# Performance work log

Hardware: AMD Instinct MI355X
Metric: run time of the kernel (lower is better)

## Reference

```python
import jax, jax.numpy as jnp
import numpy as np


def _quant(x):
    # Per-tensor dynamic uint8 quantization to produce LUT row/col indices.
    # (The CUDA kernel's exact requant scheme is not in the source; this is the
    # assumed scheme: scale so max |x| -> 255, round, clip to [0,255].)
    s = 255.0 / jnp.maximum(jnp.max(jnp.abs(x)), jnp.float32(1e-6))
    return jnp.clip(jnp.round(x * s), 0, 255).astype(jnp.int32)


def _lut_conv(x, w, b, lut):
    # CustomAnyConv2d: stride=1, padding=(2,2), kernel 5x5.
    O, Cin, kh, kw = w.shape
    # im2col patches: (B, Cin*kh*kw, H, W), feature ordering matches w.reshape(O, -1)
    patches = jax.lax.conv_general_dilated_patches(
        x, (kh, kw), (1, 1), ((2, 2), (2, 2)))
    B, K, H, W = patches.shape
    pi = _quant(patches).reshape(B, K, H * W)            # (B,K,P)
    wi = _quant(w.reshape(O, K))                          # (O,K)
    vals = lut[pi[:, None, :, :], wi[None, :, :, None]]   # (B,O,K,P) gather
    out = vals.sum(axis=2).reshape(B, O, H, W)            # accumulate LUT products
    return out + b[None, :, None, None]


def _lut_dense(x, w, b, lut):
    # CustomAnyDense: out[h, o] = sum_k LUT[x[h,k], w[o,k]] + b[o]
    xi = _quant(x)                                        # (B,K)
    wi = _quant(w)                                        # (O,K)
    vals = lut[xi[:, None, :], wi[None, :, :]]            # (B,O,K)
    return vals.sum(axis=2) + b


def _maxpool2(x, pad=0):
    return jax.lax.reduce_window(
        x, -jnp.inf, jax.lax.max,
        (1, 1, 2, 2), (1, 1, 2, 2),
        ((0, 0), (0, 0), (pad, pad), (pad, pad)))


def setup_inputs() -> dict:
    key = jax.random.key(0)
    ks = jax.random.split(key, 11)
    B = 32
    x = jax.random.uniform(ks[0], (B, 1, 28, 28), jnp.float32)
    ij = np.arange(256)
    # Approximate-multiplier LUT: high byte of exact 8x8-bit product (uint8-valued).
    lut = jnp.asarray(((ij[:, None] * ij[None, :]) >> 8).astype(np.float32))
    return {
        "x": x,
        "lut": lut,
        "w1": jax.random.uniform(ks[1], (16, 1, 5, 5), jnp.float32),
        "b1": jax.random.normal(ks[2], (16,), jnp.float32) * 0.01,
        "w2": jax.random.uniform(ks[3], (32, 16, 5, 5), jnp.float32),
        "b2": jax.random.normal(ks[4], (32,), jnp.float32) * 0.01,
        "w3": jax.random.uniform(ks[5], (64, 32, 5, 5), jnp.float32),
        "b3": jax.random.normal(ks[6], (64,), jnp.float32) * 0.01,
        "fw1": jax.random.uniform(ks[7], (256, 1024), jnp.float32),
        "fb1": jax.random.normal(ks[8], (256,), jnp.float32) * 0.01,
        "fw2": jax.random.uniform(ks[9], (10, 256), jnp.float32),
        "fb2": jax.random.normal(ks[10], (10,), jnp.float32) * 0.01,
    }


def reference(x, lut, w1, b1, w2, b2, w3, b3, fw1, fb1, fw2, fb2):
    h = jax.nn.relu(_lut_conv(x, w1, b1, lut))
    h = _maxpool2(h)                     # (B,16,14,14)
    h = jax.nn.relu(_lut_conv(h, w2, b2, lut))
    h = _maxpool2(h)                     # (B,32,7,7)
    h = jax.nn.relu(_lut_conv(h, w3, b3, lut))
    h = _maxpool2(h, pad=1)              # (B,64,4,4)
    h = h.reshape(h.shape[0], -1)        # (B,1024)
    h = jax.nn.relu(_lut_dense(h, fw1, fb1, lut))
    h = _lut_dense(h, fw2, fb2, lut)     # (B,10)
    return jax.nn.log_softmax(h, axis=1)
```

## Files before the change

### kernel.cpp

```cpp
#include <hip/hip_runtime.h>
#include <math.h>

typedef unsigned int  u32;
typedef unsigned long long u64;
typedef unsigned short u16;
typedef unsigned short u16x2 __attribute__((ext_vector_type(2)));

#define O_A1     4096
#define O_A2     405504
#define O_A3     606208
#define O_A4     737280
#define O_BARB   770048
#define BAR_WORDS 4224
#define O_FW1Q   790528

#define NBLK     512u

__device__ __forceinline__ float ldf(const float* p) {
  return __hip_atomic_load(p, __ATOMIC_RELAXED, __HIP_MEMORY_SCOPE_AGENT);
}
__device__ __forceinline__ void stf(float* p, float v) {
  __hip_atomic_store(p, v, __ATOMIC_RELAXED, __HIP_MEMORY_SCOPE_AGENT);
}
__device__ __forceinline__ u64 ld8(const u64* p) {
  return __hip_atomic_load(p, __ATOMIC_RELAXED, __HIP_MEMORY_SCOPE_AGENT);
}
__device__ __forceinline__ void st4u(u32* p, u32 v) {
  __hip_atomic_store(p, v, __ATOMIC_RELAXED, __HIP_MEMORY_SCOPE_AGENT);
}

__device__ __forceinline__ float blk_max(float v, float* red) {
  int t = threadIdx.x;
  __syncthreads();
  red[t] = v;
  __syncthreads();
#pragma unroll
  for (int s = 128; s > 0; s >>= 1) {
    if (t < s) red[t] = fmaxf(red[t], red[t + s]);
    __syncthreads();
  }
  return red[0];
}

__device__ __forceinline__ void amax_f(float* slot, float v) {
  atomicMax((int*)slot, (int)__float_as_uint(v));
}

__device__ __forceinline__ u16 quant1(float v, float s) {
  float q = rintf(v * s);
  q = fminf(fmaxf(q, 0.0f), 255.0f);
  return (u16)q;
}

__device__ __forceinline__ void mac_u32(u32& acc, u32 a, u32 w) {
  u16x2 av = __builtin_bit_cast(u16x2, a);
  u16x2 wv = __builtin_bit_cast(u16x2, w);
  u16x2 p  = av * wv;
  acc += (__builtin_bit_cast(u32, p) >> 8) & 0x00FF00FFu;
}
__device__ __forceinline__ void mac4(u32& acc, uint4 a, uint4 w) {
  mac_u32(acc, a.x, w.x); mac_u32(acc, a.y, w.y);
  mac_u32(acc, a.z, w.z); mac_u32(acc, a.w, w.w);
}

__device__ __forceinline__ float fmax4(float4 v) {
  return fmaxf(fmaxf(fabsf(v.x), fabsf(v.y)), fmaxf(fabsf(v.z), fabsf(v.w)));
}

__device__ __forceinline__ void gbar(int i, u32* bb) {
  __syncthreads();
  if (threadIdx.x == 0) {
    u32* root = bb + i * 16;
    u32* flag = bb + 64;
    u32* leaf = bb + 128 + (i * 64 + (int)(blockIdx.x >> 3)) * 16;
    asm volatile("s_waitcnt vmcnt(0)" ::: "memory");
    u32 lo = __hip_atomic_fetch_add(leaf, 1u, __ATOMIC_RELAXED,
                                    __HIP_MEMORY_SCOPE_AGENT);
    if (lo == 7u) {
      u32 ro = __hip_atomic_fetch_add(root, 1u, __ATOMIC_RELAXED,
                                      __HIP_MEMORY_SCOPE_AGENT);
      if (ro == 63u)
        __hip_atomic_store(flag, (u32)(i + 1), __ATOMIC_RELAXED,
                           __HIP_MEMORY_SCOPE_AGENT);
    }
    while (__hip_atomic_load(flag, __ATOMIC_RELAXED,
                             __HIP_MEMORY_SCOPE_AGENT) < (u32)(i + 1))
      __builtin_amdgcn_s_sleep(2);
  }
  __syncthreads();
}

__global__ __launch_bounds__(256) void k_zero(u32* p) {
  for (int i = threadIdx.x; i < BAR_WORDS; i += 256) p[i] = 0;
}

__global__ __launch_bounds__(256, 2) void k_fused(
    const float* __restrict__ x,
    const float* __restrict__ w1, const float* __restrict__ b1,
    const float* __restrict__ w2, const float* __restrict__ b2,
    const float* __restrict__ w3, const float* __restrict__ b3,
    const float* __restrict__ fw1, const float* __restrict__ fb1,
    const float* __restrict__ fw2, const float* __restrict__ fb2,
    float* __restrict__ a1, float* __restrict__ a2,
    float* __restrict__ a3, float* __restrict__ a4,
    float* __restrict__ out, float* wsf) {
  __shared__ __align__(16) union {
    struct { unsigned char sx[1024]; u16 sw[64]; } c1;
    struct { u16 sa[324 * 16]; u16 sw[800]; int sconv[196]; } c2;
    struct { u16 sa3[121 * 40]; u16 sw3[3200]; } c3;
    struct { u16 sh[1024]; } d1;
    struct { u16 sh2[256]; float z[16]; } d2;
  } sm;
  __shared__ float red[256];
  const int t = threadIdx.x, bid = blockIdx.x;
  u32* bb = (u32*)((char*)wsf + O_BARB);
  u32* fw1q32 = (u32*)((char*)wsf + O_FW1Q);

  if (bid >= 256) {
    if (bid < 315) {
      int sb = bid - 256;
      const float* p; int n4, base, nb, slot;
      if (sb < 2)       { p = w2;  n4 = 3200;  base = sb;      nb = 2;  slot = 2; }
      else if (sb < 10) { p = w3;  n4 = 12800; base = sb - 2;  nb = 8;  slot = 3; }
      else if (sb < 58) { p = fw1; n4 = 65536; base = sb - 10; nb = 48; slot = 4; }
      else              { p = fw2; n4 = 640;   base = 0;       nb = 1;  slot = 5; }
      const float4* p4 = (const float4*)p;
      float m = 0.f;
      for (int i = base * 256 + t; i < n4; i += nb * 256) m = fmaxf(m, fmax4(p4[i]));
      m = blk_max(m, red);
      if (t == 0) amax_f(wsf + slot, m);
    }
  } else {
    int b = bid >> 3, op = bid & 7;
    float m = 0.f;
    const float4* x4 = (const float4*)x;
    for (int i = t; i < 6272; i += 256) m = fmaxf(m, fmax4(x4[i]));
    float xmax = blk_max(m, red);
    m = 0.f;
    if (t < 100) m = fmax4(((const float4*)w1)[t]);
    float w1max = blk_max(m, red);
    float s0  = 255.0f / fmaxf(xmax, 1e-6f);
    float sw1 = 255.0f / fmaxf(w1max, 1e-6f);

    u32* sxz = (u32*)sm.c1.sx;
    for (int i = t; i < 256; i += 256) sxz[i] = 0;
    __syncthreads();
    for (int i = t; i < 784; i += 256) {
      int y = i / 28, xx = i - y * 28;
      sm.c1.sx[(y + 2) * 32 + xx + 2] = (unsigned char)quant1(x[b * 784 + i], s0);
    }
    if (t < 50) sm.c1.sw[t] = quant1(w1[op * 50 + t], sw1);
    __syncthreads();
    float lm = 0.f;
    if (t < 196) {
      int py = t / 14, px = t - py * 14;
#pragma unroll
      for (int ol = 0; ol < 2; ++ol) {
        int oc = op * 2 + ol;
        int best = -2147483647;
#pragma unroll
        for (int dy = 0; dy < 2; ++dy)
#pragma unroll
          for (int dx = 0; dx < 2; ++dx) {
            int cy = 2 * py + dy, cx = 2 * px + dx;
            int acc = 0;
#pragma unroll
            for (int kh = 0; kh < 5; ++kh) {
              const unsigned char* xp = sm.c1.sx + (cy + kh) * 32 + cx;
#pragma unroll
              for (int kw = 0; kw < 5; ++kw)
                acc += ((int)xp[kw] * (int)sm.c1.sw[ol * 25 + kh * 5 + kw]) >> 8;
            }
            best = max(best, acc);
          }
        float v = fmaxf(0.f, (float)best + b1[oc]);
        stf(a1 + b * 3136 + t * 16 + oc, v);
        lm = fmaxf(lm, v);
      }
    }
    lm = blk_max(lm, red);
    if (t == 0) amax_f(wsf + 6, lm);
  }
  gbar(0, bb);

  {
    {
      float swsq = 255.0f / fmaxf(ldf(wsf + 4), 1e-6f);
      int i = bid * 256 + t;
      float2 f = ((const float2*)fw1)[i];
      st4u(fw1q32 + i, (u32)quant1(f.x, swsq) | ((u32)quant1(f.y, swsq) << 16));
    }
    int b = bid >> 4, og = bid & 15;
    float s1 = 255.0f / fmaxf(ldf(wsf + 6), 1e-6f);
    float sw2s = 255.0f / fmaxf(ldf(wsf + 2), 1e-6f);
    u32* sz = (u32*)sm.c2.sa;
    for (int i = t; i < 2592; i += 256) sz[i] = 0;
    __syncthreads();
    const u64* a1u = (const u64*)(a1 + b * 3136);
    for (int i2 = t; i2 < 1568; i2 += 256) {
      int px = i2 >> 3, c2 = i2 & 7;
      int y = px / 14, xx = px - y * 14;
      float2 f = __builtin_bit_cast(float2, ld8(a1u + i2));
      u32 pk = (u32)quant1(f.x, s1) | ((u32)quant1(f.y, s1) << 16);
      ((u32*)sm.c2.sa)[((y + 2) * 18 + xx + 2) * 8 + c2] = pk;
    }
    for (int i = t; i < 800; i += 256) {
      int ol = i / 400, r = i - ol * 400, c = r / 25, tp = r - c * 25;
      sm.c2.sw[ol * 400 + tp * 16 + c] = quant1(w2[(og * 2 + ol) * 400 + c * 25 + tp], sw2s);
    }
    __syncthreads();
    int h = t & 1, pxb = t >> 1;
    float lm = 0.f;
    for (int ol = 0; ol < 2; ++ol) {
      int oc = og * 2 + ol;
      const uint4* wq = (const uint4*)(sm.c2.sw + ol * 400);
#pragma unroll
      for (int rep = 0; rep < 2; ++rep) {
        int px = pxb + rep * 128;
        if (px < 196) {
          int y = px / 14, xx = px - y * 14;
          u32 acc = 0;
#pragma unroll
          for (int kh = 0; kh < 5; ++kh)
#pragma unroll
            for (int kw = 0; kw < 5; ++kw) {
              int row = (y + kh) * 18 + (xx + kw);
              uint4 av = *(const uint4*)(sm.c2.sa + row * 16 + h * 8);
              mac4(acc, av, wq[(kh * 5 + kw) * 2 + h]);
            }
          int ai = (int)((acc & 0xFFFFu) + (acc >> 16));
          ai += __shfl_down(ai, 1, 2);
          if (h == 0) sm.c2.sconv[px] = ai;
        }
      }
      __syncthreads();
      if (t < 49) {
        int py = t / 7, px = t - py * 7;
        int mm = sm.c2.sconv[(2 * py) * 14 + 2 * px];
        mm = max(mm, sm.c2.sconv[(2 * py) * 14 + 2 * px + 1]);
        mm = max(mm, sm.c2.sconv[(2 * py + 1) * 14 + 2 * px]);
        mm = max(mm, sm.c2.sconv[(2 * py + 1) * 14 + 2 * px + 1]);
        float v = fmaxf(0.f, (float)mm + b2[oc]);
        stf(a2 + b * 1568 + t * 32 + oc, v);
        lm = fmaxf(lm, v);
      }
      __syncthreads();
    }
    lm = blk_max(lm, red);
    if (t == 0) amax_f(wsf + 7, lm);
  }
  gbar(1, bb);

  {
    int b = bid >> 4, og = bid & 15;
    float s2 = 255.0f / fmaxf(ldf(wsf + 7), 1e-6f);
    float sw3s = 255.0f / fmaxf(ldf(wsf + 3), 1e-6f);
    u32* sz = (u32*)sm.c3.sa3;
    for (int i = t; i < 2420; i += 256) sz[i] = 0;
    __syncthreads();
    const u64* a2u = (const u64*)(a2 + b * 1568);
    for (int i2 = t; i2 < 784; i2 += 256) {
      int px = i2 >> 4, c2 = i2 & 15;
      int y = px / 7, xx = px - y * 7;
      float2 f = __builtin_bit_cast(float2, ld8(a2u + i2));
      u32 pk = (u32)quant1(f.x, s2) | ((u32)quant1(f.y, s2) << 16);
      ((u32*)sm.c3.sa3)[((y + 2) * 11 + xx + 2) * 20 + c2] = pk;
    }
    for (int i = t; i < 3200; i += 256) {
      int ol = i / 800, r = i - ol * 800, c = r / 25, tp = r - c * 25;
      sm.c3.sw3[ol * 800 + tp * 32 + c] = quant1(w3[(og * 4 + ol) * 800 + c * 25 + tp], sw3s);
    }
    __syncthreads();
    int q = t & 3, pos = t >> 2;
    int dydx = pos & 3, r = pos >> 2;
    int py = r >> 2, px = r & 3;
    int cy = 2 * py - 1 + (dydx >> 1), cx = 2 * px - 1 + (dydx & 1);
    bool valid = (cy >= 0 && cy < 7 && cx >= 0 && cx < 7);
    float lm = 0.f;
    for (int ol = 0; ol < 4; ++ol) {
      int oc = og * 4 + ol;
      int ai = 0;
      if (valid) {
        u32 acc = 0;
#pragma unroll
        for (int kh = 0; kh < 5; ++kh)
#pragma unroll
          for (int kw = 0; kw < 5; ++kw) {
            int row = (cy + kh) * 11 + (cx + kw);
            uint4 av = *(const uint4*)(sm.c3.sa3 + row * 40 + q * 8);
            uint4 wv = *(const uint4*)(sm.c3.sw3 + ol * 800 + (kh * 5 + kw) * 32 + q * 8);
            mac4(acc, av, wv);
          }
        ai = (int)((acc & 0xFFFFu) + (acc >> 16));
      }
      ai += __shfl_down(ai, 2, 4);
      ai += __shfl_down(ai, 1, 4);
      int val = valid ? ai : -(1 << 30);
      int mm = max(val, __shfl_down(val, 4, 16));
      mm = max(mm, __shfl_down(mm, 8, 16));
      if ((t & 15) == 0) {
        float v = fmaxf(0.f, (float)mm + b3[oc]);
        stf(a3 + b * 1024 + oc * 16 + r, v);
        lm = fmaxf(lm, v);
      }
    }
    lm = blk_max(lm, red);
    if (t == 0) amax_f(wsf + 8, lm);
  }
  gbar(2, bb);

  {
    int b = bid >> 4, og = bid & 15;
    float s3 = 255.0f / fmaxf(ldf(wsf + 8), 1e-6f);
    const u64* a3u = (const u64*)(a3 + b * 1024);
    for (int i2 = t; i2 < 512; i2 += 256) {
      float2 f = __builtin_bit_cast(float2, ld8(a3u + i2));
      ((u32*)sm.d1.sh)[i2] = (u32)quant1(f.x, s3) | ((u32)quant1(f.y, s3) << 16);
    }
    __syncthreads();
    int ol = t >> 4, ks = t & 15;
    int o = og * 16 + ol;
    const u64* wq8 = (const u64*)fw1q32 + o * 256;
    const uint4* hp = (const uint4*)sm.d1.sh;
    u32 acc = 0;
#pragma unroll
    for (int j = 0; j < 8; ++j) {
      int e = j * 16 + ks;
      u64 w01 = ld8(wq8 + e * 2), w23 = ld8(wq8 + e * 2 + 1);
      uint4 wv;
      wv.x = (u32)w01; wv.y = (u32)(w01 >> 32);
      wv.z = (u32)w23; wv.w = (u32)(w23 >> 32);
      mac4(acc, hp[e], wv);
    }
    int ai = (int)((acc & 0xFFFFu) + (acc >> 16));
#pragma unroll
    for (int d = 8; d > 0; d >>= 1)
      ai += __shfl_down(ai, d, 16);
    float lm = 0.f;
    if (ks == 0) {
      float v = fmaxf(0.f, (float)ai + fb1[o]);
      stf(a4 + b * 256 + o, v);
      lm = v;
    }
    lm = blk_max(lm, red);
    if (t == 0) amax_f(wsf + 9, lm);
  }
  gbar(3, bb);

  if (bid < 32) {
    int b = bid;
    float s4 = 255.0f / fmaxf(ldf(wsf + 9), 1e-6f);
    float sws = 255.0f / fmaxf(ldf(wsf + 5), 1e-6f);
    sm.d2.sh2[t] = quant1(ldf(a4 + b * 256 + t), s4);
    __syncthreads();
    if (t < 40) {
      int o = t >> 2, ks = t & 3;
      const float4* wf = (const float4*)(fw2 + o * 256);
      const uint4* hp = (const uint4*)sm.d2.sh2;
      u32 acc = 0;
#pragma unroll
      for (int j = 0; j < 8; ++j) {
        int e = j * 4 + ks;
        float4 f0 = wf[e * 2], f1 = wf[e * 2 + 1];
        uint4 wv;
        wv.x = (u32)quant1(f0.x, sws) | ((u32)quant1(f0.y, sws) << 16);
        wv.y = (u32)quant1(f0.z, sws) | ((u32)quant1(f0.w, sws) << 16);
        wv.z = (u32)quant1(f1.x, sws) | ((u32)quant1(f1.y, sws) << 16);
        wv.w = (u32)quant1(f1.z, sws) | ((u32)quant1(f1.w, sws) << 16);
        mac4(acc, hp[e], wv);
      }
      int ai = (int)((acc & 0xFFFFu) + (acc >> 16));
      ai += __shfl_down(ai, 2, 4);
      ai += __shfl_down(ai, 1, 4);
      if (ks == 0) sm.d2.z[o] = (float)ai + fb2[o];
    }
    __syncthreads();
    if (t < 10) {
      float mz = sm.d2.z[0];
#pragma unroll
      for (int j = 1; j < 10; ++j) mz = fmaxf(mz, sm.d2.z[j]);
      float se = 0.f;
#pragma unroll
      for (int j = 0; j < 10; ++j) se += expf(sm.d2.z[j] - mz);
      out[b * 10 + t] = sm.d2.z[t] - (mz + logf(se));
    }
  }
}

extern "C" void kernel_launch(void* const* d_in, const int* in_sizes, int n_in,
                              void* d_out, int out_size, void* d_ws, size_t ws_size,
                              hipStream_t stream) {
  const float* x   = (const float*)d_in[0];
  const float* w1  = (const float*)d_in[2];
  const float* b1  = (const float*)d_in[3];
  const float* w2  = (const float*)d_in[4];
  const float* b2  = (const float*)d_in[5];
  const float* w3  = (const float*)d_in[6];
  const float* b3  = (const float*)d_in[7];
  const float* fw1 = (const float*)d_in[8];
  const float* fb1 = (const float*)d_in[9];
  const float* fw2 = (const float*)d_in[10];
  const float* fb2 = (const float*)d_in[11];
  float* out = (float*)d_out;
  unsigned char* ws8 = (unsigned char*)d_ws;
  float* wsf = (float*)d_ws;
  float* A1 = (float*)(ws8 + O_A1);
  float* A2 = (float*)(ws8 + O_A2);
  float* A3 = (float*)(ws8 + O_A3);
  float* A4 = (float*)(ws8 + O_A4);
  u32* barp = (u32*)(ws8 + O_BARB);

  k_zero<<<1, 256, 0, stream>>>(barp);
  k_fused<<<512, 256, 0, stream>>>(x, w1, b1, w2, b2, w3, b3,
                                   fw1, fb1, fw2, fb2,
                                   A1, A2, A3, A4, out, wsf);
}
```

Baseline: 140.7 us.

## Double persistent grid to 1024 blocks and halve per-block output channels

Grows the fused persistent kernel from 512 to 1024 blocks, with launch bounds raised to 4 blocks per CU so the whole grid can be co-resident. Each stage's per-block channel work is halved: conv1 does one channel, conv2 one, conv3 two, and dense1 eight outputs with a 32-lane reduction. The hierarchical grid barrier is widened to 128 leaves. The goal is more parallelism and latency hiding across all CUs. The cost is twice as many blocks hitting barrier atomics, repeated per-block staging of input activations, and register pressure from the tighter occupancy bound.

```diff
diff --git a/kernel.cpp b/kernel.cpp
--- a/kernel.cpp
+++ b/kernel.cpp
@@ -11,10 +11,10 @@
 #define O_A3     606208
 #define O_A4     737280
 #define O_BARB   770048
-#define BAR_WORDS 4224
-#define O_FW1Q   790528
-
-#define NBLK     512u
+#define BAR_WORDS 8320
+#define O_FW1Q   803328
+
+#define NBLK     1024u
 
 __device__ __forceinline__ float ldf(const float* p) {
   return __hip_atomic_load(p, __ATOMIC_RELAXED, __HIP_MEMORY_SCOPE_AGENT);
@@ -72,14 +72,14 @@
   if (threadIdx.x == 0) {
     u32* root = bb + i * 16;
     u32* flag = bb + 64;
-    u32* leaf = bb + 128 + (i * 64 + (int)(blockIdx.x >> 3)) * 16;
+    u32* leaf = bb + 128 + (i * 128 + (int)(blockIdx.x >> 3)) * 16;
     asm volatile("s_waitcnt vmcnt(0)" ::: "memory");
     u32 lo = __hip_atomic_fetch_add(leaf, 1u, __ATOMIC_RELAXED,
                                     __HIP_MEMORY_SCOPE_AGENT);
     if (lo == 7u) {
       u32 ro = __hip_atomic_fetch_add(root, 1u, __ATOMIC_RELAXED,
                                       __HIP_MEMORY_SCOPE_AGENT);
-      if (ro == 63u)
+      if (ro == 127u)
         __hip_atomic_store(flag, (u32)(i + 1), __ATOMIC_RELAXED,
                            __HIP_MEMORY_SCOPE_AGENT);
     }
@@ -94,7 +94,7 @@
   for (int i = threadIdx.x; i < BAR_WORDS; i += 256) p[i] = 0;
 }
 
-__global__ __launch_bounds__(256, 2) void k_fused(
+__global__ __launch_bounds__(256, 4) void k_fused(
     const float* __restrict__ x,
     const float* __restrict__ w1, const float* __restrict__ b1,
     const float* __restrict__ w2, const float* __restrict__ b2,
@@ -116,22 +116,8 @@
   u32* bb = (u32*)((char*)wsf + O_BARB);
   u32* fw1q32 = (u32*)((char*)wsf + O_FW1Q);
 
-  if (bid >= 256) {
-    if (bid < 315) {
-      int sb = bid - 256;
-      const float* p; int n4, base, nb, slot;
-      if (sb < 2)       { p = w2;  n4 = 3200;  base = sb;      nb = 2;  slot = 2; }
-      else if (sb < 10) { p = w3;  n4 = 12800; base = sb - 2;  nb = 8;  slot = 3; }
-      else if (sb < 58) { p = fw1; n4 = 65536; base = sb - 10; nb = 48; slot = 4; }
-      else              { p = fw2; n4 = 640;   base = 0;       nb = 1;  slot = 5; }
-      const float4* p4 = (const float4*)p;
-      float m = 0.f;
-      for (int i = base * 256 + t; i < n4; i += nb * 256) m = fmaxf(m, fmax4(p4[i]));
-      m = blk_max(m, red);
-      if (t == 0) amax_f(wsf + slot, m);
-    }
-  } else {
-    int b = bid >> 3, op = bid & 7;
+  if (bid < 512) {
+    int b = bid >> 4, op = bid & 15;
     float m = 0.f;
     const float4* x4 = (const float4*)x;
     for (int i = t; i < 6272; i += 256) m = fmaxf(m, fmax4(x4[i]));
@@ -149,48 +135,56 @@
       int y = i / 28, xx = i - y * 28;
       sm.c1.sx[(y + 2) * 32 + xx + 2] = (unsigned char)quant1(x[b * 784 + i], s0);
     }
-    if (t < 50) sm.c1.sw[t] = quant1(w1[op * 50 + t], sw1);
+    if (t < 25) sm.c1.sw[t] = quant1(w1[op * 25 + t], sw1);
     __syncthreads();
     float lm = 0.f;
     if (t < 196) {
       int py = t / 14, px = t - py * 14;
-#pragma unroll
-      for (int ol = 0; ol < 2; ++ol) {
-        int oc = op * 2 + ol;
-        int best = -2147483647;
-#pragma unroll
-        for (int dy = 0; dy < 2; ++dy)
-#pragma unroll
-          for (int dx = 0; dx < 2; ++dx) {
-            int cy = 2 * py + dy, cx = 2 * px + dx;
-            int acc = 0;
-#pragma unroll
-            for (int kh = 0; kh < 5; ++kh) {
-              const unsigned char* xp = sm.c1.sx + (cy + kh) * 32 + cx;
-#pragma unroll
-              for (int kw = 0; kw < 5; ++kw)
-                acc += ((int)xp[kw] * (int)sm.c1.sw[ol * 25 + kh * 5 + kw]) >> 8;
-            }
-            best = max(best, acc);
+      int best = -2147483647;
+#pragma unroll
+      for (int dy = 0; dy < 2; ++dy)
+#pragma unroll
+        for (int dx = 0; dx < 2; ++dx) {
+          int cy = 2 * py + dy, cx = 2 * px + dx;
+          int acc = 0;
+#pragma unroll
+          for (int kh = 0; kh < 5; ++kh) {
+            const unsigned char* xp = sm.c1.sx + (cy + kh) * 32 + cx;
+#pragma unroll
+            for (int kw = 0; kw < 5; ++kw)
+              acc += ((int)xp[kw] * (int)sm.c1.sw[kh * 5 + kw]) >> 8;
           }
-        float v = fmaxf(0.f, (float)best + b1[oc]);
-        stf(a1 + b * 3136 + t * 16 + oc, v);
-        lm = fmaxf(lm, v);
-      }
+          best = max(best, acc);
+        }
+      float v = fmaxf(0.f, (float)best + b1[op]);
+      stf(a1 + b * 3136 + t * 16 + op, v);
+      lm = v;
     }
     lm = blk_max(lm, red);
     if (t == 0) amax_f(wsf + 6, lm);
+  } else if (bid < 571) {
+    int sb = bid - 512;
+    const float* p; int n4, base, nb, slot;
+    if (sb < 2)       { p = w2;  n4 = 3200;  base = sb;      nb = 2;  slot = 2; }
+    else if (sb < 10) { p = w3;  n4 = 12800; base = sb - 2;  nb = 8;  slot = 3; }
+    else if (sb < 58) { p = fw1; n4 = 65536; base = sb - 10; nb = 48; slot = 4; }
+    else              { p = fw2; n4 = 640;   base = 0;       nb = 1;  slot = 5; }
+    const float4* p4 = (const float4*)p;
+    float m = 0.f;
+    for (int i = base * 256 + t; i < n4; i += nb * 256) m = fmaxf(m, fmax4(p4[i]));
+    m = blk_max(m, red);
+    if (t == 0) amax_f(wsf + slot, m);
   }
   gbar(0, bb);
 
   {
-    {
+    if (t < 128) {
       float swsq = 255.0f / fmaxf(ldf(wsf + 4), 1e-6f);
-      int i = bid * 256 + t;
+      int i = bid * 128 + t;
       float2 f = ((const float2*)fw1)[i];
       st4u(fw1q32 + i, (u32)quant1(f.x, swsq) | ((u32)quant1(f.y, swsq) << 16));
     }
-    int b = bid >> 4, og = bid & 15;
+    int b = bid >> 5, oc = bid & 31;
     float s1 = 255.0f / fmaxf(ldf(wsf + 6), 1e-6f);
     float sw2s = 255.0f / fmaxf(ldf(wsf + 2), 1e-6f);
     u32* sz = (u32*)sm.c2.sa;
@@ -204,47 +198,43 @@
       u32 pk = (u32)quant1(f.x, s1) | ((u32)quant1(f.y, s1) << 16);
       ((u32*)sm.c2.sa)[((y + 2) * 18 + xx + 2) * 8 + c2] = pk;
     }
-    for (int i = t; i < 800; i += 256) {
-      int ol = i / 400, r = i - ol * 400, c = r / 25, tp = r - c * 25;
-      sm.c2.sw[ol * 400 + tp * 16 + c] = quant1(w2[(og * 2 + ol) * 400 + c * 25 + tp], sw2s);
+    for (int i = t; i < 400; i += 256) {
+      int c = i / 25, tp = i - c * 25;
+      sm.c2.sw[tp * 16 + c] = quant1(w2[oc * 400 + c * 25 + tp], sw2s);
     }
     __syncthreads();
     int h = t & 1, pxb = t >> 1;
     float lm = 0.f;
-    for (int ol = 0; ol < 2; ++ol) {
-      int oc = og * 2 + ol;
-      const uint4* wq = (const uint4*)(sm.c2.sw + ol * 400);
-#pragma unroll
-      for (int rep = 0; rep < 2; ++rep) {
-        int px = pxb + rep * 128;
-        if (px < 196) {
-          int y = px / 14, xx = px - y * 14;
-          u32 acc = 0;
-#pragma unroll
-          for (int kh = 0; kh < 5; ++kh)
-#pragma unroll
-            for (int kw = 0; kw < 5; ++kw) {
-              int row = (y + kh) * 18 + (xx + kw);
-              uint4 av = *(const uint4*)(sm.c2.sa + row * 16 + h * 8);
-              mac4(acc, av, wq[(kh * 5 + kw) * 2 + h]);
-            }
-          int ai = (int)((acc & 0xFFFFu) + (acc >> 16));
-          ai += __shfl_down(ai, 1, 2);
-          if (h == 0) sm.c2.sconv[px] = ai;
-        }
+    const uint4* wq = (const uint4*)sm.c2.sw;
+#pragma unroll
+    for (int rep = 0; rep < 2; ++rep) {
+      int px = pxb + rep * 128;
+      if (px < 196) {
+        int y = px / 14, xx = px - y * 14;
+        u32 acc = 0;
+#pragma unroll
+        for (int kh = 0; kh < 5; ++kh)
+#pragma unroll
+          for (int kw = 0; kw < 5; ++kw) {
+            int row = (y + kh) * 18 + (xx + kw);
+            uint4 av = *(const uint4*)(sm.c2.sa + row * 16 + h * 8);
+            mac4(acc, av, wq[(kh * 5 + kw) * 2 + h]);
+          }
+        int ai = (int)((acc & 0xFFFFu) + (acc >> 16));
+        ai += __shfl_down(ai, 1, 2);
+        if (h == 0) sm.c2.sconv[px] = ai;
       }
-      __syncthreads();
-      if (t < 49) {
-        int py = t / 7, px = t - py * 7;
-        int mm = sm.c2.sconv[(2 * py) * 14 + 2 * px];
-        mm = max(mm, sm.c2.sconv[(2 * py) * 14 + 2 * px + 1]);
-        mm = max(mm, sm.c2.sconv[(2 * py + 1) * 14 + 2 * px]);
-        mm = max(mm, sm.c2.sconv[(2 * py + 1) * 14 + 2 * px + 1]);
-        float v = fmaxf(0.f, (float)mm + b2[oc]);
-        stf(a2 + b * 1568 + t * 32 + oc, v);
-        lm = fmaxf(lm, v);
-      }
-      __syncthreads();
+    }
+    __syncthreads();
+    if (t < 49) {
+      int py = t / 7, px = t - py * 7;
+      int mm = sm.c2.sconv[(2 * py) * 14 + 2 * px];
+      mm = max(mm, sm.c2.sconv[(2 * py) * 14 + 2 * px + 1]);
+      mm = max(mm, sm.c2.sconv[(2 * py + 1) * 14 + 2 * px]);
+      mm = max(mm, sm.c2.sconv[(2 * py + 1) * 14 + 2 * px + 1]);
+      float v = fmaxf(0.f, (float)mm + b2[oc]);
+      stf(a2 + b * 1568 + t * 32 + oc, v);
+      lm = v;
     }
     lm = blk_max(lm, red);
     if (t == 0) amax_f(wsf + 7, lm);
@@ -252,7 +242,7 @@
   gbar(1, bb);
 
   {
-    int b = bid >> 4, og = bid & 15;
+    int b = bid >> 5, ocg = bid & 31;
     float s2 = 255.0f / fmaxf(ldf(wsf + 7), 1e-6f);
     float sw3s = 255.0f / fmaxf(ldf(wsf + 3), 1e-6f);
     u32* sz = (u32*)sm.c3.sa3;
@@ -266,9 +256,9 @@
       u32 pk = (u32)quant1(f.x, s2) | ((u32)quant1(f.y, s2) << 16);
       ((u32*)sm.c3.sa3)[((y + 2) * 11 + xx + 2) * 20 + c2] = pk;
     }
-    for (int i = t; i < 3200; i += 256) {
+    for (int i = t; i < 1600; i += 256) {
       int ol = i / 800, r = i - ol * 800, c = r / 25, tp = r - c * 25;
-      sm.c3.sw3[ol * 800 + tp * 32 + c] = quant1(w3[(og * 4 + ol) * 800 + c * 25 + tp], sw3s);
+      sm.c3.sw3[ol * 800 + tp * 32 + c] = quant1(w3[(ocg * 2 + ol) * 800 + c * 25 + tp], sw3s);
     }
     __syncthreads();
     int q = t & 3, pos = t >> 2;
@@ -277,8 +267,8 @@
     int cy = 2 * py - 1 + (dydx >> 1), cx = 2 * px - 1 + (dydx & 1);
     bool valid = (cy >= 0 && cy < 7 && cx >= 0 && cx < 7);
     float lm = 0.f;
-    for (int ol = 0; ol < 4; ++ol) {
-      int oc = og * 4 + ol;
+    for (int ol = 0; ol < 2; ++ol) {
+      int oc = ocg * 2 + ol;
       int ai = 0;
       if (valid) {
         u32 acc = 0;
@@ -310,7 +300,7 @@
   gbar(2, bb);
 
   {
-    int b = bid >> 4, og = bid & 15;
+    int b = bid >> 5, og = bid & 31;
     float s3 = 255.0f / fmaxf(ldf(wsf + 8), 1e-6f);
     const u64* a3u = (const u64*)(a3 + b * 1024);
     for (int i2 = t; i2 < 512; i2 += 256) {
@@ -318,14 +308,14 @@
       ((u32*)sm.d1.sh)[i2] = (u32)quant1(f.x, s3) | ((u32)quant1(f.y, s3) << 16);
     }
     __syncthreads();
-    int ol = t >> 4, ks = t & 15;
-    int o = og * 16 + ol;
+    int ol = t >> 5, ks = t & 31;
+    int o = og * 8 + ol;
     const u64* wq8 = (const u64*)fw1q32 + o * 256;
     const uint4* hp = (const uint4*)sm.d1.sh;
     u32 acc = 0;
 #pragma unroll
-    for (int j = 0; j < 8; ++j) {
-      int e = j * 16 + ks;
+    for (int j = 0; j < 4; ++j) {
+      int e = j * 32 + ks;
       u64 w01 = ld8(wq8 + e * 2), w23 = ld8(wq8 + e * 2 + 1);
       uint4 wv;
       wv.x = (u32)w01; wv.y = (u32)(w01 >> 32);
@@ -334,8 +324,8 @@
     }
     int ai = (int)((acc & 0xFFFFu) + (acc >> 16));
 #pragma unroll
-    for (int d = 8; d > 0; d >>= 1)
-      ai += __shfl_down(ai, d, 16);
+    for (int d = 16; d > 0; d >>= 1)
+      ai += __shfl_down(ai, d, 32);
     float lm = 0.f;
     if (ks == 0) {
       float v = fmaxf(0.f, (float)ai + fb1[o]);
@@ -411,7 +401,7 @@
   u32* barp = (u32*)(ws8 + O_BARB);
 
   k_zero<<<1, 256, 0, stream>>>(barp);
-  k_fused<<<512, 256, 0, stream>>>(x, w1, b1, w2, b2, w3, b3,
-                                   fw1, fb1, fw2, fb2,
-                                   A1, A2, A3, A4, out, wsf);
-}
+  k_fused<<<1024, 256, 0, stream>>>(x, w1, b1, w2, b2, w3, b3,
+                                    fw1, fb1, fw2, fb2,
+                                    A1, A2, A3, A4, out, wsf);
+}
```

Result: slower. 155.0 us (+10.2%).
